# Performance work log

Hardware: AMD Instinct MI355X
Metric: run time of the kernel (lower is better)

The kernel has to match this reference:

```python
import jax, jax.numpy as jnp
import numpy as np

N_NODES = 100000
N_EDGES = 300000
D_IN = 256
D_OUT = 256
NEG_SLOPE = 0.2


def setup_inputs() -> dict:
    key = jax.random.key(0)
    ks = jax.random.split(key, 6)
    feat = jax.random.normal(ks[0], (N_NODES, D_IN), dtype=jnp.float32)
    # xavier-normal-ish init scale
    scale = (2.0 / (D_IN + D_OUT)) ** 0.5
    W_src = jax.random.normal(ks[1], (D_IN, D_OUT), dtype=jnp.float32) * scale
    b_src = jnp.zeros((D_OUT,), dtype=jnp.float32)
    W_dst = jax.random.normal(ks[2], (D_IN, D_OUT), dtype=jnp.float32) * scale
    b_dst = jnp.zeros((D_OUT,), dtype=jnp.float32)
    attn = jax.random.normal(ks[3], (D_OUT,), dtype=jnp.float32) * scale
    src = jax.random.randint(ks[4], (N_EDGES,), 0, N_NODES, dtype=jnp.int32)
    dst = jax.random.randint(ks[5], (N_EDGES,), 0, N_NODES, dtype=jnp.int32)
    return {"feat": feat, "W_src": W_src, "b_src": b_src,
            "W_dst": W_dst, "b_dst": b_dst, "attn": attn,
            "src": src, "dst": dst}


def reference(feat, W_src, b_src, W_dst, b_dst, attn, src, dst):
    N = feat.shape[0]
    # node projections (dense GEMMs)
    el = feat @ W_src + b_src          # [N, D_OUT]  (feat_src / 'el')
    er = feat @ W_dst + b_dst          # [N, D_OUT]  (feat_dst / 'er')
    # edge-wise u_add_v + LeakyReLU, then attention dot
    e = jax.nn.leaky_relu(el[src] + er[dst], NEG_SLOPE)  # [E, D_OUT]
    score = e @ attn                    # [E]  ((e*attn).sum(-1))
    # edge softmax segmented by destination node
    smax = jax.ops.segment_max(score, dst, num_segments=N)   # [N]
    ex = jnp.exp(score - smax[dst])                           # [E]
    ssum = jax.ops.segment_sum(ex, dst, num_segments=N)      # [N]
    a = ex / ssum[dst]                                        # [E]
    # weighted scatter-sum aggregation: u_mul_e('el','a') -> sum per dst
    out = jax.ops.segment_sum(el[src] * a[:, None], dst, num_segments=N)
    return out  # [N, D_OUT]
```

## Files before the change

### kernel.cpp

```cpp
#include <hip/hip_runtime.h>
#include <cstdint>
#include <cmath>

#define D 256
#define NEG 0.2f
#define BK 64

typedef __attribute__((ext_vector_type(8))) __bf16 bf16x8;
typedef __attribute__((ext_vector_type(8))) unsigned short ushort8;
typedef __attribute__((ext_vector_type(4))) float f32x4;

__device__ __forceinline__ unsigned short f2bf(float f){
    unsigned u = __float_as_uint(f);
    return (unsigned short)((u + 0x7fffu + ((u >> 16) & 1u)) >> 16);
}
__device__ __forceinline__ float b2f(unsigned short u){
    return __uint_as_float(((unsigned)u) << 16);
}

__device__ __forceinline__ void gload_lds16(const void* g, void* l){
    __builtin_amdgcn_global_load_lds(
        (const __attribute__((address_space(1))) unsigned int*)g,
        (__attribute__((address_space(3))) unsigned int*)l, 16, 0, 0);
}

__global__ __launch_bounds__(256) void prep_w_kernel(
    const float* __restrict__ Wsrc, const float* __restrict__ Wdst,
    const float* __restrict__ bsrc, const float* __restrict__ bdst,
    unsigned short* __restrict__ WT, float* __restrict__ biascat)
{
    int idx = blockIdx.x*256 + threadIdx.x;
    int col = idx >> 5;
    int u   = idx & 31;
    int gu  = (u & 24) | ((u ^ col) & 7);
    const float* W = (col < 256) ? Wsrc : Wdst;
    int c = col & 255;
    ushort8 o;
    #pragma unroll
    for (int j = 0; j < 8; ++j)
        o[j] = f2bf(W[(size_t)(gu*8 + j)*D + c]);
    *(ushort8*)(WT + (size_t)col*D + u*8) = o;
    if (idx < 512) biascat[idx] = (idx < 256) ? bsrc[idx] : bdst[idx-256];
}

__global__ __launch_bounds__(256) void prep_feat_kernel(
    const float* __restrict__ feat, unsigned short* __restrict__ featb, int N, int NPAD)
{
    int total = NPAD * 32;
    for (int idx = blockIdx.x*256 + threadIdx.x; idx < total; idx += gridDim.x*256){
        int r = idx >> 5;
        int u = idx & 31;
        ushort8 o;
        if (r < N){
            int gu = (u & 24) | ((u ^ r) & 7);
            const float* s = feat + (size_t)r*D + gu*8;
            float4 a = *(const float4*)s;
            float4 b = *(const float4*)(s + 4);
            o[0]=f2bf(a.x); o[1]=f2bf(a.y); o[2]=f2bf(a.z); o[3]=f2bf(a.w);
            o[4]=f2bf(b.x); o[5]=f2bf(b.y); o[6]=f2bf(b.z); o[7]=f2bf(b.w);
        } else {
            #pragma unroll
            for (int j = 0; j < 8; ++j) o[j] = 0;
        }
        *(ushort8*)(featb + (size_t)r*D + u*8) = o;
    }
}

__global__ __launch_bounds__(256) void proj_mfma_kernel(
    const unsigned short* __restrict__ featb, const unsigned short* __restrict__ WT,
    const float* __restrict__ biascat,
    unsigned short* __restrict__ el16, unsigned short* __restrict__ er16, int N)
{
    __shared__ unsigned short As[128*BK];
    __shared__ unsigned short Bs[128*BK];

    const int tid  = threadIdx.x;
    const int wave = tid >> 6;
    const int lane = tid & 63;
    const int col0 = blockIdx.x * 128;
    const int row0 = blockIdx.y * 128;
    const int wr = (wave >> 1) * 64;
    const int wc = (wave & 1) * 64;
    const int l15 = lane & 15;
    const int kg  = lane >> 4;

    const int sr = (wave << 3) + (lane >> 3);
    const int sc = (lane & 7) * 8;

    f32x4 acc[4][4] = {};

    for (int k0 = 0; k0 < D; k0 += BK) {
        #pragma unroll
        for (int r4 = 0; r4 < 4; ++r4) {
            int ar = r4*32 + sr;
            gload_lds16(featb + (size_t)(row0 + ar)*D + k0 + sc,
                        &As[(r4*32 + wave*8)*BK]);
            gload_lds16(WT + (size_t)(col0 + ar)*D + k0 + sc,
                        &Bs[(r4*32 + wave*8)*BK]);
        }
        __syncthreads();

        #pragma unroll
        for (int ks = 0; ks < 2; ++ks) {
            bf16x8 af[4], bfr[4];
            #pragma unroll
            for (int m = 0; m < 4; ++m){
                int row = wr + m*16 + l15;
                int c = ((kg + ks*4) ^ (row & 7)) * 8;
                af[m] = *(const bf16x8*)&As[row*BK + c];
            }
            #pragma unroll
            for (int n = 0; n < 4; ++n){
                int row = wc + n*16 + l15;
                int c = ((kg + ks*4) ^ (row & 7)) * 8;
                bfr[n] = *(const bf16x8*)&Bs[row*BK + c];
            }
            #pragma unroll
            for (int m = 0; m < 4; ++m)
                #pragma unroll
                for (int n = 0; n < 4; ++n)
                    acc[m][n] = __builtin_amdgcn_mfma_f32_16x16x32_bf16(bfr[n], af[m], acc[m][n], 0, 0, 0);
        }
        __syncthreads();
    }

    unsigned short* __restrict__ dstp = (col0 < 256) ? el16 : er16;
    const int ccbase = col0 & 255;
    #pragma unroll
    for (int m = 0; m < 4; ++m) {
        int row = row0 + wr + m*16 + l15;
        if (row >= N) continue;
        #pragma unroll
        for (int n = 0; n < 4; ++n) {
            int cw = wc + n*16 + kg*4;
            float4 b4 = *(const float4*)(biascat + col0 + cw);
            ushort4 o;
            o.x = f2bf(acc[m][n][0] + b4.x);
            o.y = f2bf(acc[m][n][1] + b4.y);
            o.z = f2bf(acc[m][n][2] + b4.z);
            o.w = f2bf(acc[m][n][3] + b4.w);
            *(ushort4*)(dstp + (size_t)row*D + ccbase + cw) = o;
        }
    }
}

__global__ void count_kernel(const int* __restrict__ dst, int* __restrict__ deg, int E){
    int e = blockIdx.x*blockDim.x + threadIdx.x;
    if (e < E) atomicAdd(&deg[dst[e]], 1);
}

__global__ __launch_bounds__(256) void scan1_kernel(const int* __restrict__ deg,
                                                    int* __restrict__ incl,
                                                    int* __restrict__ bsum, int N){
    __shared__ int s[256];
    int i = blockIdx.x*256 + threadIdx.x;
    int v = (i < N) ? deg[i] : 0;
    s[threadIdx.x] = v;
    __syncthreads();
    #pragma unroll
    for (int off = 1; off < 256; off <<= 1){
        int t = (threadIdx.x >= off) ? s[threadIdx.x - off] : 0;
        __syncthreads();
        s[threadIdx.x] += t;
        __syncthreads();
    }
    if (i < N) incl[i] = s[threadIdx.x];
    if (threadIdx.x == 255) bsum[blockIdx.x] = s[255];
}

__global__ __launch_bounds__(512) void scan2_kernel(int* __restrict__ bsum, int nb){
    __shared__ int s[512];
    int t = threadIdx.x;
    int v = (t < nb) ? bsum[t] : 0;
    s[t] = v;
    __syncthreads();
    #pragma unroll
    for (int off = 1; off < 512; off <<= 1){
        int u = (t >= off) ? s[t - off] : 0;
        __syncthreads();
        s[t] += u;
        __syncthreads();
    }
    if (t < nb) bsum[t] = s[t] - v;
}

__global__ __launch_bounds__(256) void scan3_kernel(const int* __restrict__ deg,
                                                    const int* __restrict__ incl,
                                                    const int* __restrict__ bsum,
                                                    int* __restrict__ rowstart,
                                                    int* __restrict__ cursor, int N){
    int i = blockIdx.x*256 + threadIdx.x;
    if (i < N){
        int st = incl[i] - deg[i] + bsum[blockIdx.x];
        rowstart[i] = st;
        cursor[i]   = st;
    }
}

__global__ void scatter_kernel(const int* __restrict__ dst, int* __restrict__ cursor,
                               int* __restrict__ eid, int E){
    int e = blockIdx.x*blockDim.x + threadIdx.x;
    if (e < E){
        int pos = atomicAdd(&cursor[dst[e]], 1);
        eid[pos] = e;
    }
}

__global__ __launch_bounds__(256) void gat_node_kernel(
    const unsigned short* __restrict__ el16, const unsigned short* __restrict__ er16,
    const float* __restrict__ attn, const int* __restrict__ src,
    const int* __restrict__ eid, const int* __restrict__ rowstart,
    const int* __restrict__ degv, float* __restrict__ out, int N)
{
    int node = blockIdx.x*4 + (threadIdx.x >> 6);
    if (node >= N) return;
    int lane = threadIdx.x & 63;
    float4 o = make_float4(0.f,0.f,0.f,0.f);
    int deg = degv[node];
    float* op = out + (size_t)node*D + lane*4;
    if (deg == 0){ *(float4*)op = o; return; }

    ushort4 rv = *(const ushort4*)(er16 + (size_t)node*D + lane*4);
    float4 r4 = make_float4(b2f(rv.x), b2f(rv.y), b2f(rv.z), b2f(rv.w));
    float4 a4 = *(const float4*)(attn + lane*4);
    int start = rowstart[node];

    float m = -INFINITY, ssum = 0.f;
    for (int k = 0; k < deg; ++k){
        int e  = eid[start + k];
        int sn = src[e];
        ushort4 lv = *(const ushort4*)(el16 + (size_t)sn*D + lane*4);
        float4 l4 = make_float4(b2f(lv.x), b2f(lv.y), b2f(lv.z), b2f(lv.w));
        float x, p = 0.f;
        x = l4.x + r4.x; p += (x > 0.f ? x : NEG*x) * a4.x;
        x = l4.y + r4.y; p += (x > 0.f ? x : NEG*x) * a4.y;
        x = l4.z + r4.z; p += (x > 0.f ? x : NEG*x) * a4.z;
        x = l4.w + r4.w; p += (x > 0.f ? x : NEG*x) * a4.w;
        #pragma unroll
        for (int off = 32; off > 0; off >>= 1) p += __shfl_xor(p, off, 64);
        float newm  = fmaxf(m, p);
        float scale = __expf(m - newm);
        float w     = __expf(p - newm);
        ssum = ssum*scale + w;
        o.x = o.x*scale + w*l4.x;
        o.y = o.y*scale + w*l4.y;
        o.z = o.z*scale + w*l4.z;
        o.w = o.w*scale + w*l4.w;
        m = newm;
    }
    float inv = 1.f/ssum;
    o.x *= inv; o.y *= inv; o.z *= inv; o.w *= inv;
    *(float4*)op = o;
}

extern "C" void kernel_launch(void* const* d_in, const int* in_sizes, int n_in,
                              void* d_out, int out_size, void* d_ws, size_t ws_size,
                              hipStream_t stream)
{
    const float* feat = (const float*)d_in[0];
    const float* Wsrc = (const float*)d_in[1];
    const float* bsrc = (const float*)d_in[2];
    const float* Wdst = (const float*)d_in[3];
    const float* bdst = (const float*)d_in[4];
    const float* attn = (const float*)d_in[5];
    const int*   src  = (const int*)d_in[6];
    const int*   dst  = (const int*)d_in[7];
    const int N = in_sizes[0] / D;
    const int E = in_sizes[6];
    const int NPAD = ((N + 127)/128)*128;
    float* out = (float*)d_out;

    unsigned short* el16 = (unsigned short*)d_ws;
    unsigned short* er16 = el16 + (size_t)N*D;
    int* deg      = (int*)(er16 + (size_t)N*D);
    int* incl     = deg + N;
    int* rowstart = incl + N;
    int* cursor   = rowstart + N;
    int* bsum     = cursor + N;
    int* eid      = bsum + 512;
    unsigned short* WT = (unsigned short*)(eid + E);
    float* biascat = (float*)(WT + (size_t)512*D);
    unsigned short* featb = (unsigned short*)(biascat + 512);

    const int nb = (N + 255)/256;

    hipMemsetAsync(deg, 0, (size_t)N*sizeof(int), stream);

    prep_w_kernel<<<64, 256, 0, stream>>>(Wsrc, Wdst, bsrc, bdst, WT, biascat);
    prep_feat_kernel<<<4096, 256, 0, stream>>>(feat, featb, N, NPAD);

    dim3 pgrid(4, NPAD/128);
    proj_mfma_kernel<<<pgrid, 256, 0, stream>>>(featb, WT, biascat, el16, er16, N);

    count_kernel<<<(E + 255)/256, 256, 0, stream>>>(dst, deg, E);
    scan1_kernel<<<nb, 256, 0, stream>>>(deg, incl, bsum, N);
    scan2_kernel<<<1, 512, 0, stream>>>(bsum, nb);
    scan3_kernel<<<nb, 256, 0, stream>>>(deg, incl, bsum, rowstart, cursor, N);
    scatter_kernel<<<(E + 255)/256, 256, 0, stream>>>(dst, cursor, eid, E);

    gat_node_kernel<<<(N + 3)/4, 256, 0, stream>>>(el16, er16, attn, src, eid,
                                                   rowstart, deg, out, N);
}
```

Measured before the change: 214.0 us.

## Store source ids in CSR and batch four edge gathers per iteration

The scatter step now writes the source node id directly into the CSR array instead of the edge id, which removes one dependent indirection (eid then src) from the per-edge gather. The node kernel processes edges in groups of four: it issues four el row loads up front, computes four partial scores, and interleaves their wave reductions before the sequential online-softmax updates. This is meant to expose more memory-level parallelism and cut load latency chains in the aggregation kernel. The cost is higher register use and redundant loads when a node's degree is not a multiple of four.

```diff
diff --git a/kernel.cpp b/kernel.cpp
--- a/kernel.cpp
+++ b/kernel.cpp
@@ -197,20 +197,20 @@
     }
 }
 
-__global__ void scatter_kernel(const int* __restrict__ dst, int* __restrict__ cursor,
-                               int* __restrict__ eid, int E){
+__global__ void scatter_kernel(const int* __restrict__ dst, const int* __restrict__ src,
+                               int* __restrict__ cursor, int* __restrict__ srcs, int E){
     int e = blockIdx.x*blockDim.x + threadIdx.x;
     if (e < E){
         int pos = atomicAdd(&cursor[dst[e]], 1);
-        eid[pos] = e;
+        srcs[pos] = src[e];
     }
 }
 
 __global__ __launch_bounds__(256) void gat_node_kernel(
     const unsigned short* __restrict__ el16, const unsigned short* __restrict__ er16,
-    const float* __restrict__ attn, const int* __restrict__ src,
-    const int* __restrict__ eid, const int* __restrict__ rowstart,
-    const int* __restrict__ degv, float* __restrict__ out, int N)
+    const float* __restrict__ attn, const int* __restrict__ srcs,
+    const int* __restrict__ rowstart, const int* __restrict__ degv,
+    float* __restrict__ out, int N)
 {
     int node = blockIdx.x*4 + (threadIdx.x >> 6);
     if (node >= N) return;
@@ -226,27 +226,43 @@
     int start = rowstart[node];
 
     float m = -INFINITY, ssum = 0.f;
-    for (int k = 0; k < deg; ++k){
-        int e  = eid[start + k];
-        int sn = src[e];
-        ushort4 lv = *(const ushort4*)(el16 + (size_t)sn*D + lane*4);
-        float4 l4 = make_float4(b2f(lv.x), b2f(lv.y), b2f(lv.z), b2f(lv.w));
-        float x, p = 0.f;
-        x = l4.x + r4.x; p += (x > 0.f ? x : NEG*x) * a4.x;
-        x = l4.y + r4.y; p += (x > 0.f ? x : NEG*x) * a4.y;
-        x = l4.z + r4.z; p += (x > 0.f ? x : NEG*x) * a4.z;
-        x = l4.w + r4.w; p += (x > 0.f ? x : NEG*x) * a4.w;
-        #pragma unroll
-        for (int off = 32; off > 0; off >>= 1) p += __shfl_xor(p, off, 64);
-        float newm  = fmaxf(m, p);
-        float scale = __expf(m - newm);
-        float w     = __expf(p - newm);
-        ssum = ssum*scale + w;
-        o.x = o.x*scale + w*l4.x;
-        o.y = o.y*scale + w*l4.y;
-        o.z = o.z*scale + w*l4.z;
-        o.w = o.w*scale + w*l4.w;
-        m = newm;
+    for (int base = 0; base < deg; base += 4){
+        int cnt = deg - base; if (cnt > 4) cnt = 4;
+        float4 l[4]; float p[4];
+        #pragma unroll
+        for (int j = 0; j < 4; ++j){
+            int k = base + j; if (k >= deg) k = deg - 1;
+            int sn = srcs[start + k];
+            ushort4 lv = *(const ushort4*)(el16 + (size_t)sn*D + lane*4);
+            l[j] = make_float4(b2f(lv.x), b2f(lv.y), b2f(lv.z), b2f(lv.w));
+        }
+        #pragma unroll
+        for (int j = 0; j < 4; ++j){
+            float x, pp = 0.f;
+            x = l[j].x + r4.x; pp += (x > 0.f ? x : NEG*x) * a4.x;
+            x = l[j].y + r4.y; pp += (x > 0.f ? x : NEG*x) * a4.y;
+            x = l[j].z + r4.z; pp += (x > 0.f ? x : NEG*x) * a4.z;
+            x = l[j].w + r4.w; pp += (x > 0.f ? x : NEG*x) * a4.w;
+            p[j] = pp;
+        }
+        #pragma unroll
+        for (int off = 32; off > 0; off >>= 1){
+            #pragma unroll
+            for (int j = 0; j < 4; ++j) p[j] += __shfl_xor(p[j], off, 64);
+        }
+        #pragma unroll
+        for (int j = 0; j < 4; ++j){
+            if (j >= cnt) break;
+            float newm  = fmaxf(m, p[j]);
+            float scale = __expf(m - newm);
+            float w     = __expf(p[j] - newm);
+            ssum = ssum*scale + w;
+            o.x = o.x*scale + w*l[j].x;
+            o.y = o.y*scale + w*l[j].y;
+            o.z = o.z*scale + w*l[j].z;
+            o.w = o.w*scale + w*l[j].w;
+            m = newm;
+        }
     }
     float inv = 1.f/ssum;
     o.x *= inv; o.y *= inv; o.z *= inv; o.w *= inv;
@@ -277,8 +293,8 @@
     int* rowstart = incl + N;
     int* cursor   = rowstart + N;
     int* bsum     = cursor + N;
-    int* eid      = bsum + 512;
-    unsigned short* WT = (unsigned short*)(eid + E);
+    int* srcs     = bsum + 512;
+    unsigned short* WT = (unsigned short*)(srcs + E);
     float* biascat = (float*)(WT + (size_t)512*D);
     unsigned short* featb = (unsigned short*)(biascat + 512);
 
@@ -296,8 +312,8 @@
     scan1_kernel<<<nb, 256, 0, stream>>>(deg, incl, bsum, N);
     scan2_kernel<<<1, 512, 0, stream>>>(bsum, nb);
     scan3_kernel<<<nb, 256, 0, stream>>>(deg, incl, bsum, rowstart, cursor, N);
-    scatter_kernel<<<(E + 255)/256, 256, 0, stream>>>(dst, cursor, eid, E);
-
-    gat_node_kernel<<<(N + 3)/4, 256, 0, stream>>>(el16, er16, attn, src, eid,
+    scatter_kernel<<<(E + 255)/256, 256, 0, stream>>>(dst, src, cursor, srcs, E);
+
+    gat_node_kernel<<<(N + 3)/4, 256, 0, stream>>>(el16, er16, attn, srcs,
                                                    rowstart, deg, out, N);
 }
```

Measured after the change: 189.6 us. 11.4% less time.
